# Kernel optimization log

Hardware: AMD Instinct MI355X
Metric: run time of the kernel (lower is better)

The kernel has to match this reference:

```python
import jax, jax.numpy as jnp
import numpy as np

H, W = 48, 48
L = H * W            # 2304 tokens
D = 256              # d_model
NH = 8               # heads (self and memory attn)
FF = 1024            # dim_feedforward
T = 2                # memory frames
BS = 1
GN_GROUPS = 32       # GNActDWConv2d default groups


def layernorm(x, g, b, eps=1e-5):
    m = jnp.mean(x, -1, keepdims=True)
    v = jnp.mean((x - m) ** 2, -1, keepdims=True)
    return (x - m) * jax.lax.rsqrt(v + eps) * g + b


def linear(x, Wt, b):
    # torch nn.Linear convention: Wt is [out, in]
    return x @ Wt.T + b


def mha_core(Q, K, V, nhead):
    # Q [Lq, bs, C], K/V [Lk, bs, C]; AOT MultiheadAttention core (eval: no dropout)
    Lq, bs, C = Q.shape
    hd = C // nhead
    Qh = (Q / np.float32(np.sqrt(hd))).reshape(Lq, bs, nhead, hd).transpose(1, 2, 0, 3)
    Kh = K.reshape(-1, bs, nhead, hd).transpose(1, 2, 0, 3)
    Vh = V.reshape(-1, bs, nhead, hd).transpose(1, 2, 0, 3)
    attn = jax.nn.softmax(jnp.einsum('bhqd,bhkd->bhqk', Qh, Kh), axis=-1)
    out = jnp.einsum('bhqk,bhkd->bhqd', attn, Vh)
    return out.transpose(2, 0, 1, 3).reshape(Lq, bs, C)


def groupnorm(x, g, b, groups, eps=1e-5):
    bs, c, h, w = x.shape
    xg = x.reshape(bs, groups, c // groups, h, w)
    m = jnp.mean(xg, (2, 3, 4), keepdims=True)
    v = jnp.mean((xg - m) ** 2, (2, 3, 4), keepdims=True)
    xg = (xg - m) * jax.lax.rsqrt(v + eps)
    return xg.reshape(bs, c, h, w) * g[None, :, None, None] + b[None, :, None, None]


def dwconv5(x, k):
    # depthwise 5x5, padding=2; x [bs,c,h,w], k [c,1,5,5]
    return jax.lax.conv_general_dilated(x, k, (1, 1), ((2, 2), (2, 2)),
                                        feature_group_count=x.shape[1])


def setup_inputs() -> dict:
    key = jax.random.key(0)
    ks = jax.random.split(key, 16)
    rn = lambda i, shape, s=1.0: jax.random.normal(ks[i], shape, jnp.float32) * s
    w = 0.02
    inp = {
        'tgt': rn(0, (L, BS, D)),
        'global_K': rn(1, (T, L, BS, D)),
        'global_V': rn(2, (T, L, BS, D)),
        'local_K': rn(3, (L, BS, D)),
        'local_V': rn(4, (L, BS, D)),
        # LayerNorms
        'ln1_g': jnp.ones(D, jnp.float32), 'ln1_b': jnp.zeros(D, jnp.float32),
        'ln2_g': jnp.ones(D, jnp.float32), 'ln2_b': jnp.zeros(D, jnp.float32),
        'ln3_g': jnp.ones(D, jnp.float32), 'ln3_b': jnp.zeros(D, jnp.float32),
        'ln4_g': jnp.ones(D, jnp.float32), 'ln4_b': jnp.zeros(D, jnp.float32),
        # self_attn (use_linear=True) Q/K/V + projection
        'sa_Wq': rn(5, (D, D), w), 'sa_bq': jnp.zeros(D, jnp.float32),
        'sa_Wk': rn(6, (D, D), w), 'sa_bk': jnp.zeros(D, jnp.float32),
        'sa_Wv': rn(7, (D, D), w), 'sa_bv': jnp.zeros(D, jnp.float32),
        'sa_Wo': rn(8, (D, D), w), 'sa_bo': jnp.zeros(D, jnp.float32),
        # block linear_Q
        'Wq': rn(9, (D, D), w), 'bq': jnp.zeros(D, jnp.float32),
        # long/short term attn projections (use_linear=False)
        'lt_Wo': rn(10, (D, D), w), 'lt_bo': jnp.zeros(D, jnp.float32),
        'st_Wo': rn(11, (D, D), w), 'st_bo': jnp.zeros(D, jnp.float32),
        # FFN: linear1 -> GN+GELU+DWConv -> linear2
        'W1': rn(12, (FF, D), w), 'b1': jnp.zeros(FF, jnp.float32),
        'gn_g': jnp.ones(FF, jnp.float32), 'gn_b': jnp.zeros(FF, jnp.float32),
        'dw_k': rn(13, (FF, 1, 5, 5), 0.05),
        'W2': rn(14, (D, FF), w), 'b2': jnp.zeros(D, jnp.float32),
    }
    return inp


def reference(tgt, global_K, global_V, local_K, local_V,
              ln1_g, ln1_b, ln2_g, ln2_b, ln3_g, ln3_b, ln4_g, ln4_b,
              sa_Wq, sa_bq, sa_Wk, sa_bk, sa_Wv, sa_bv, sa_Wo, sa_bo,
              Wq, bq, lt_Wo, lt_bo, st_Wo, st_bo,
              W1, b1, gn_g, gn_b, dw_k, W2, b2):
    # --- stage 1: self-attention ---
    _tgt = layernorm(tgt, ln1_g, ln1_b)
    q = linear(_tgt, sa_Wq, sa_bq)
    k = linear(_tgt, sa_Wk, sa_bk)
    v = linear(_tgt, sa_Wv, sa_bv)
    tgt2 = linear(mha_core(q, k, v, NH), sa_Wo, sa_bo)
    tgt = tgt + tgt2  # droppath is identity at eval

    # --- stage 2: long-term + short-term memory cross-attention ---
    _tgt = layernorm(tgt, ln2_g, ln2_b)
    curr_Q = linear(_tgt, Wq, bq)
    curr_K = curr_Q
    curr_V = _tgt

    flat_K = global_K.reshape(-1, BS, D)  # [T*L, bs, D]
    flat_V = global_V.reshape(-1, BS, D)
    tgt2 = linear(mha_core(curr_Q, flat_K, flat_V, NH), lt_Wo, lt_bo)

    k_st = layernorm(local_K + curr_K, ln4_g, ln4_b)
    v_st = layernorm(local_V + curr_V, ln4_g, ln4_b)
    tgt3 = linear(mha_core(curr_Q, k_st, v_st, NH), st_Wo, st_bo)

    tgt = tgt + tgt2 + tgt3

    # --- stage 3: FFN with GN + GELU + depthwise conv ---
    _tgt = layernorm(tgt, ln3_g, ln3_b)
    x = linear(_tgt, W1, b1)                        # [L, bs, FF]
    x = x.reshape(H, W, BS, FF).transpose(2, 3, 0, 1)  # [bs, FF, H, W]
    x = jax.nn.gelu(groupnorm(x, gn_g, gn_b, GN_GROUPS), approximate=False)
    x = dwconv5(x, dw_k)
    x = x.reshape(BS, FF, L).transpose(2, 0, 1)     # [L, bs, FF]
    tgt2 = linear(x, W2, b2)
    return tgt + tgt2
```

## Files before the change

kernel.cpp:

```cpp
#include <hip/hip_runtime.h>
#include <hip/hip_bf16.h>

#define L   2304
#define D   256
#define NHD 8
#define HD  32
#define FF  1024
#define HH  48
#define WWW 48
#define SPL 4
#define RCH 24
#define RP  (L / RCH)
#define S2LOG 0.25503486f

typedef unsigned short bfraw;
typedef __attribute__((ext_vector_type(8))) short s8v;
typedef __attribute__((ext_vector_type(4))) float f4v;

__device__ __forceinline__ bfraw f2b(float x) {
    __hip_bfloat16 h = __float2bfloat16(x);
    return __builtin_bit_cast(bfraw, h);
}

__global__ __launch_bounds__(256) void diag_kernel(float* __restrict__ out, float c, int n)
{
    int i = blockIdx.x * 256 + threadIdx.x;
    if (i < n) out[i] = c;
}

__global__ __launch_bounds__(256) void ln_kernel(
    const float* __restrict__ inA, const float* __restrict__ inB,
    const float* __restrict__ g, const float* __restrict__ b,
    float* __restrict__ out, bfraw* __restrict__ outb)
{
    int row = blockIdx.x, t = threadIdx.x;
    size_t idx = (size_t)row * D + t;
    float v = inA[idx];
    if (inB) v += inB[idx];
    __shared__ float rs[256], rq[256];
    rs[t] = v; rq[t] = v * v;
    __syncthreads();
    for (int o = 128; o > 0; o >>= 1) {
        if (t < o) { rs[t] += rs[t + o]; rq[t] += rq[t + o]; }
        __syncthreads();
    }
    float mean = rs[0] * (1.f / D);
    float var  = rq[0] * (1.f / D) - mean * mean;
    float rstd = rsqrtf(var + 1e-5f);
    float r = (v - mean) * rstd * g[t] + b[t];
    if (out)  out[idx]  = r;
    if (outb) outb[idx] = f2b(r);
}

__global__ __launch_bounds__(256) void ln2_ln4v(
    const float* __restrict__ t5, const float* __restrict__ lV,
    const float* __restrict__ g2, const float* __restrict__ b2,
    const float* __restrict__ g4, const float* __restrict__ b4,
    bfraw* __restrict__ out2b, float* __restrict__ outv)
{
    int row = blockIdx.x, t = threadIdx.x;
    size_t idx = (size_t)row * D + t;
    float v = t5[idx];
    __shared__ float rs[256], rq[256];
    rs[t] = v; rq[t] = v * v;
    __syncthreads();
    for (int o = 128; o > 0; o >>= 1) {
        if (t < o) { rs[t] += rs[t + o]; rq[t] += rq[t + o]; }
        __syncthreads();
    }
    float mean = rs[0] * (1.f / D);
    float var  = rq[0] * (1.f / D) - mean * mean;
    float rstd = rsqrtf(var + 1e-5f);
    float r2 = (v - mean) * rstd * g2[t] + b2[t];
    out2b[idx] = f2b(r2);
    float u = r2 + lV[idx];
    __syncthreads();
    rs[t] = u; rq[t] = u * u;
    __syncthreads();
    for (int o = 128; o > 0; o >>= 1) {
        if (t < o) { rs[t] += rs[t + o]; rq[t] += rq[t + o]; }
        __syncthreads();
    }
    float mean2 = rs[0] * (1.f / D);
    float var2  = rq[0] * (1.f / D) - mean2 * mean2;
    float rstd2 = rsqrtf(var2 + 1e-5f);
    outv[idx] = (u - mean2) * rstd2 * g4[t] + b4[t];
}

__global__ __launch_bounds__(256) void gemm_mfma(
    const bfraw* __restrict__ A, const float* __restrict__ W,
    const float* __restrict__ bias, const float* res, float* out,
    bfraw* __restrict__ outb, float oscale,
    int M, int N, int K)
{
    __shared__ __attribute__((aligned(16))) short Wl[64][32];
    int t = threadIdx.x;
    int w = t >> 6, l = t & 63;
    int lo = l & 15, quad = l >> 4;
    int m0 = blockIdx.x * 32, n0 = blockIdx.y * 64;
    int wr = (w & 1) * 16, wc = (w >> 1) * 32;
    f4v acc[2];
    acc[0] = (f4v){0.f, 0.f, 0.f, 0.f};
    acc[1] = (f4v){0.f, 0.f, 0.f, 0.f};

    int aswz = (quad ^ ((lo >> 2) & 3)) * 8;
    int srow = t >> 3, spart = t & 7;
    const bfraw* ap = A + (size_t)(m0 + wr + lo) * K + quad * 8;

    for (int k0 = 0; k0 < K; k0 += 32) {
        float4 w4[2];
        #pragma unroll
        for (int i = 0; i < 2; i++)
            w4[i] = *reinterpret_cast<const float4*>(W + (size_t)(n0 + i * 32 + srow) * K + k0 + spart * 4);
        s8v af = *reinterpret_cast<const s8v*>(ap + k0);
        __syncthreads();
        #pragma unroll
        for (int i = 0; i < 2; i++) {
            int row = i * 32 + srow;
            int col = ((spart >> 1) ^ ((row >> 2) & 3)) * 8 + (spart & 1) * 4;
            ushort4 wb;
            wb.x = f2b(w4[i].x); wb.y = f2b(w4[i].y); wb.z = f2b(w4[i].z); wb.w = f2b(w4[i].w);
            *reinterpret_cast<ushort4*>(&Wl[row][col]) = wb;
        }
        __syncthreads();
        #pragma unroll
        for (int j = 0; j < 2; j++) {
            int rw = wc + j * 16 + lo;
            s8v wf = *reinterpret_cast<const s8v*>(&Wl[rw][aswz]);
            acc[j] = __builtin_amdgcn_mfma_f32_16x16x32_bf16(af, wf, acc[j], 0, 0, 0);
        }
    }

    #pragma unroll
    for (int j = 0; j < 2; j++) {
        #pragma unroll
        for (int r = 0; r < 4; r++) {
            int mrow = m0 + wr + quad * 4 + r;
            int ncol = n0 + wc + j * 16 + lo;
            float v = acc[j][r] + bias[ncol];
            size_t idx = (size_t)mrow * N + ncol;
            if (res) v += res[idx];
            if (out) out[idx] = v;
            if (outb) outb[idx] = f2b(v * oscale);
        }
    }
}

__global__ __launch_bounds__(256) void gemm_qkv(
    const bfraw* __restrict__ A,
    const float* __restrict__ Wq_, const float* __restrict__ bq_,
    const float* __restrict__ Wk_, const float* __restrict__ bk_,
    const float* __restrict__ Wv_, const float* __restrict__ bv_,
    bfraw* __restrict__ qb, bfraw* __restrict__ kb, bfraw* __restrict__ vtb)
{
    __shared__ __attribute__((aligned(16))) short Wl[64][32];
    int t = threadIdx.x;
    int w = t >> 6, l = t & 63;
    int lo = l & 15, quad = l >> 4;
    int sel = blockIdx.y >> 2;
    int m0 = blockIdx.x * 32, n0 = (blockIdx.y & 3) * 64;
    int wr = (w & 1) * 16, wc = (w >> 1) * 32;
    const float* W    = (sel == 0) ? Wq_ : (sel == 1) ? Wk_ : Wv_;
    const float* bias = (sel == 0) ? bq_ : (sel == 1) ? bk_ : bv_;
    f4v acc[2];
    acc[0] = (f4v){0.f, 0.f, 0.f, 0.f};
    acc[1] = (f4v){0.f, 0.f, 0.f, 0.f};

    int aswz = (quad ^ ((lo >> 2) & 3)) * 8;
    int srow = t >> 3, spart = t & 7;
    const bfraw* ap = A + (size_t)(m0 + wr + lo) * D + quad * 8;

    for (int k0 = 0; k0 < D; k0 += 32) {
        float4 w4[2];
        #pragma unroll
        for (int i = 0; i < 2; i++)
            w4[i] = *reinterpret_cast<const float4*>(W + (size_t)(n0 + i * 32 + srow) * D + k0 + spart * 4);
        s8v af = *reinterpret_cast<const s8v*>(ap + k0);
        __syncthreads();
        #pragma unroll
        for (int i = 0; i < 2; i++) {
            int row = i * 32 + srow;
            int col = ((spart >> 1) ^ ((row >> 2) & 3)) * 8 + (spart & 1) * 4;
            ushort4 wb;
            wb.x = f2b(w4[i].x); wb.y = f2b(w4[i].y); wb.z = f2b(w4[i].z); wb.w = f2b(w4[i].w);
            *reinterpret_cast<ushort4*>(&Wl[row][col]) = wb;
        }
        __syncthreads();
        #pragma unroll
        for (int j = 0; j < 2; j++) {
            int rw = wc + j * 16 + lo;
            s8v wf = *reinterpret_cast<const s8v*>(&Wl[rw][aswz]);
            acc[j] = __builtin_amdgcn_mfma_f32_16x16x32_bf16(af, wf, acc[j], 0, 0, 0);
        }
    }

    #pragma unroll
    for (int j = 0; j < 2; j++) {
        #pragma unroll
        for (int r = 0; r < 4; r++) {
            int mrow = m0 + wr + quad * 4 + r;
            int ncol = n0 + wc + j * 16 + lo;
            float v = acc[j][r] + bias[ncol];
            if (sel == 0)      qb[(size_t)mrow * D + ncol] = f2b(v * S2LOG);
            else if (sel == 1) kb[(size_t)mrow * D + ncol] = f2b(v);
            else               vtb[(size_t)ncol * L + mrow] = f2b(v);
        }
    }
}

__global__ __launch_bounds__(256) void cvtT_kernel(
    const float* __restrict__ in, bfraw* __restrict__ out, int N)
{
    __shared__ float Ls[32][33];
    int h = blockIdx.y, n0 = blockIdx.x * 32, t = threadIdx.x;
    int nl = t >> 3, dq = t & 7;
    float4 v = *reinterpret_cast<const float4*>(in + (size_t)(n0 + nl) * D + h * HD + dq * 4);
    Ls[nl][dq*4+0] = v.x; Ls[nl][dq*4+1] = v.y;
    Ls[nl][dq*4+2] = v.z; Ls[nl][dq*4+3] = v.w;
    __syncthreads();
    int dl = t >> 3, nq = t & 7;
    ushort4 o;
    o.x = f2b(Ls[nq*4+0][dl]); o.y = f2b(Ls[nq*4+1][dl]);
    o.z = f2b(Ls[nq*4+2][dl]); o.w = f2b(Ls[nq*4+3][dl]);
    *reinterpret_cast<ushort4*>(out + (size_t)(h * HD + dl) * N + n0 + nq * 4) = o;
}

__global__ __launch_bounds__(256) void cvt_both(
    const float* __restrict__ gK, bfraw* __restrict__ kb1,
    const float* __restrict__ gV, bfraw* __restrict__ vtb1)
{
    __shared__ float Ls[32][33];
    int t = threadIdx.x;
    if (blockIdx.y < NHD) {
        int h = blockIdx.y, n0 = blockIdx.x * 32;
        const int N = 2 * L;
        int nl = t >> 3, dq = t & 7;
        float4 v = *reinterpret_cast<const float4*>(gV + (size_t)(n0 + nl) * D + h * HD + dq * 4);
        Ls[nl][dq*4+0] = v.x; Ls[nl][dq*4+1] = v.y;
        Ls[nl][dq*4+2] = v.z; Ls[nl][dq*4+3] = v.w;
        __syncthreads();
        int dl = t >> 3, nq = t & 7;
        ushort4 o;
        o.x = f2b(Ls[nq*4+0][dl]); o.y = f2b(Ls[nq*4+1][dl]);
        o.z = f2b(Ls[nq*4+2][dl]); o.w = f2b(Ls[nq*4+3][dl]);
        *reinterpret_cast<ushort4*>(vtb1 + (size_t)(h * HD + dl) * N + n0 + nq * 4) = o;
    } else {
        size_t i = ((size_t)(blockIdx.x * 8 + (blockIdx.y - NHD)) * 256 + t) * 4;
        float4 v = *reinterpret_cast<const float4*>(gK + i);
        ushort4 o;
        o.x = f2b(v.x); o.y = f2b(v.y); o.z = f2b(v.z); o.w = f2b(v.w);
        *reinterpret_cast<ushort4*>(kb1 + i) = o;
    }
}

__global__ __launch_bounds__(256) void attn_mfma_split(
    const bfraw* __restrict__ Qb, const bfraw* __restrict__ Kb,
    const bfraw* __restrict__ Vt, float* __restrict__ OP,
    float* __restrict__ ML, int Lk, int chunk)
{
    __shared__ __attribute__((aligned(16))) short Ks[64][32];
    __shared__ __attribute__((aligned(16))) short Vts[32][72];
    __shared__ __attribute__((aligned(16))) short Ps[4][16][72];
    __shared__ float Tb[4][16][33];
    int t = threadIdx.x;
    int w = t >> 6, l = t & 63;
    int h = blockIdx.y, q0 = blockIdx.x * 64 + w * 16, z = blockIdx.z;
    int lo = l & 15, quad = l >> 4;
    int kb = z * chunk, ke = kb + chunk;

    s8v qf = *reinterpret_cast<const s8v*>(Qb + (size_t)(q0 + lo) * D + h * HD + quad * 8);
    int kswz = (quad ^ ((lo >> 2) & 3)) * 8;

    int skey = t >> 2, spart = t & 3;
    int kcol = (spart ^ ((skey >> 2) & 3)) * 8;
    int sd = t >> 3, svp = t & 7;
    const bfraw* kp = Kb + (size_t)skey * D + h * HD + spart * 8;
    const bfraw* vp = Vt + (size_t)(h * HD + sd) * Lk + svp * 8;

    float m_r = -1e30f, l_r = 0.f;
    f4v o0 = {0.f, 0.f, 0.f, 0.f}, o1 = {0.f, 0.f, 0.f, 0.f};

    for (int k0 = kb; k0 < ke; k0 += 64) {
        s8v kv = *reinterpret_cast<const s8v*>(kp + (size_t)k0 * D);
        s8v vv = *reinterpret_cast<const s8v*>(vp + k0);
        __syncthreads();
        *reinterpret_cast<s8v*>(&Ks[skey][kcol]) = kv;
        *reinterpret_cast<s8v*>(&Vts[sd][svp * 8]) = vv;
        __syncthreads();

        f4v sc4[4];
        #pragma unroll
        for (int s = 0; s < 4; s++) {
            s8v kf = *reinterpret_cast<const s8v*>(&Ks[lo + 16 * s][kswz]);
            sc4[s] = __builtin_amdgcn_mfma_f32_16x16x32_bf16(kf, qf, (f4v){0.f,0.f,0.f,0.f}, 0, 0, 0);
        }
        float cm = -1e30f;
        #pragma unroll
        for (int s = 0; s < 4; s++)
            #pragma unroll
            for (int r = 0; r < 4; r++)
                cm = fmaxf(cm, sc4[s][r]);
        cm = fmaxf(cm, __shfl_xor(cm, 16));
        cm = fmaxf(cm, __shfl_xor(cm, 32));
        bool skip = __all(cm <= m_r + 8.f);
        if (!skip) {
            float mnew = fmaxf(m_r, cm);
            float alpha = __builtin_amdgcn_exp2f(m_r - mnew);
            l_r *= alpha;
            #pragma unroll
            for (int r = 0; r < 4; r++) { o0[r] *= alpha; o1[r] *= alpha; }
            m_r = mnew;
        }
        float ls = 0.f;
        #pragma unroll
        for (int s = 0; s < 4; s++) {
            float p0 = __builtin_amdgcn_exp2f(sc4[s][0] - m_r);
            float p1 = __builtin_amdgcn_exp2f(sc4[s][1] - m_r);
            float p2 = __builtin_amdgcn_exp2f(sc4[s][2] - m_r);
            float p3 = __builtin_amdgcn_exp2f(sc4[s][3] - m_r);
            ls += p0 + p1 + p2 + p3;
            ushort4 pk;
            pk.x = f2b(p0); pk.y = f2b(p1); pk.z = f2b(p2); pk.w = f2b(p3);
            *reinterpret_cast<ushort4*>(&Ps[w][lo][s * 16 + quad * 4]) = pk;
        }
        ls += __shfl_xor(ls, 16);
        ls += __shfl_xor(ls, 32);
        l_r += ls;
        #pragma unroll
        for (int kc = 0; kc < 2; kc++) {
            s8v pf = *reinterpret_cast<const s8v*>(&Ps[w][lo][kc * 32 + quad * 8]);
            s8v v0 = *reinterpret_cast<const s8v*>(&Vts[lo][kc * 32 + quad * 8]);
            s8v v1 = *reinterpret_cast<const s8v*>(&Vts[16 + lo][kc * 32 + quad * 8]);
            o0 = __builtin_amdgcn_mfma_f32_16x16x32_bf16(v0, pf, o0, 0, 0, 0);
            o1 = __builtin_amdgcn_mfma_f32_16x16x32_bf16(v1, pf, o1, 0, 0, 0);
        }
    }

    #pragma unroll
    for (int r = 0; r < 4; r++) {
        Tb[w][lo][quad * 4 + r]      = o0[r];
        Tb[w][lo][16 + quad * 4 + r] = o1[r];
    }
    float* Oz = OP + (size_t)z * L * D;
    int ql = l >> 2, dq = (l & 3) * 8;
    float4 u0, u1;
    u0.x = Tb[w][ql][dq + 0]; u0.y = Tb[w][ql][dq + 1];
    u0.z = Tb[w][ql][dq + 2]; u0.w = Tb[w][ql][dq + 3];
    u1.x = Tb[w][ql][dq + 4]; u1.y = Tb[w][ql][dq + 5];
    u1.z = Tb[w][ql][dq + 6]; u1.w = Tb[w][ql][dq + 7];
    *reinterpret_cast<float4*>(Oz + (size_t)(q0 + ql) * D + h * HD + dq)     = u0;
    *reinterpret_cast<float4*>(Oz + (size_t)(q0 + ql) * D + h * HD + dq + 4) = u1;
    if (l < 16) {
        size_t mi = (((size_t)z * NHD + h) * L + q0 + lo) * 2;
        ML[mi]     = m_r;
        ML[mi + 1] = l_r;
    }
}

__global__ __launch_bounds__(256) void attn_combine(
    const float* __restrict__ OP, const float* __restrict__ ML,
    bfraw* __restrict__ Ob)
{
    int q = blockIdx.x, t = threadIdx.x, h = t >> 5;
    float m[SPL], lv[SPL];
    float M = -1e30f;
    #pragma unroll
    for (int s = 0; s < SPL; s++) {
        size_t mi = (((size_t)s * NHD + h) * L + q) * 2;
        m[s]  = ML[mi];
        lv[s] = ML[mi + 1];
        M = fmaxf(M, m[s]);
    }
    float wl = 0.f, acc = 0.f;
    #pragma unroll
    for (int s = 0; s < SPL; s++) {
        float w = __builtin_amdgcn_exp2f(m[s] - M);
        wl  += w * lv[s];
        acc += w * OP[(size_t)s * L * D + (size_t)q * D + t];
    }
    Ob[(size_t)q * D + t] = f2b(acc / wl);
}

__global__ __launch_bounds__(256) void gn_stats_part(
    const float* __restrict__ X, float* __restrict__ ps)
{
    int g = blockIdx.x, rc = blockIdx.y, t = threadIdx.x;
    int cq = (t & 7) * 4;
    int rl = t >> 3;
    int r0 = rc * RP;
    float s = 0.f, sq = 0.f;
    #pragma unroll
    for (int p = 0; p < RP / 32; p++) {
        int l = r0 + p * 32 + rl;
        float4 v = *reinterpret_cast<const float4*>(X + (size_t)l * FF + g * 32 + cq);
        s  += v.x + v.y + v.z + v.w;
        sq += v.x*v.x + v.y*v.y + v.z*v.z + v.w*v.w;
    }
    __shared__ float rs[256], rq[256];
    rs[t] = s; rq[t] = sq;
    __syncthreads();
    for (int o = 128; o > 0; o >>= 1) {
        if (t < o) { rs[t] += rs[t + o]; rq[t] += rq[t + o]; }
        __syncthreads();
    }
    if (t == 0) {
        ps[(g * RCH + rc) * 2]     = rs[0];
        ps[(g * RCH + rc) * 2 + 1] = rq[0];
    }
}

__global__ __launch_bounds__(256) void gn_gelu_dwconv(
    const float* __restrict__ X, const float* __restrict__ ps,
    const float* __restrict__ gg, const float* __restrict__ gb,
    const float* __restrict__ Kw, bfraw* __restrict__ Y)
{
    __shared__ float tile[144][64];
    int h0 = blockIdx.x * 8, w0 = blockIdx.y * 8, c0 = blockIdx.z * 64;
    int t = threadIdx.x;
    int c = t & 63;
    int cg = (c0 + c) >> 5;
    float s = 0.f, sq = 0.f;
    #pragma unroll
    for (int i = 0; i < RCH; i++) {
        s  += ps[(cg * RCH + i) * 2];
        sq += ps[(cg * RCH + i) * 2 + 1];
    }
    float n = (float)(L * 32);
    float mu = s / n;
    float rs = rsqrtf(sq / n - mu * mu + 1e-5f);
    float ga = gg[c0 + c], be = gb[c0 + c];

    for (int i = t; i < 144 * 64; i += 256) {
        int sp = i >> 6;
        int hy = h0 + (sp / 12) - 2, wx = w0 + (sp % 12) - 2;
        float v = 0.f;
        if (hy >= 0 && hy < HH && wx >= 0 && wx < WWW) {
            float x = X[(size_t)(hy * WWW + wx) * FF + c0 + c];
            x = (x - mu) * rs * ga + be;
            v = 0.5f * x * (1.f + erff(x * 0.70710678118654752f));
        }
        tile[sp][c] = v;
    }
    float kw[25];
    #pragma unroll
    for (int i = 0; i < 25; i++) kw[i] = Kw[(size_t)(c0 + c) * 25 + i];
    __syncthreads();

    int sgrp = t >> 6;
    for (int sIdx = 0; sIdx < 16; sIdx++) {
        int sp = sgrp * 16 + sIdx;
        int oh = sp >> 3, ow = sp & 7;
        float acc = 0.f;
        #pragma unroll
        for (int ky = 0; ky < 5; ky++)
            #pragma unroll
            for (int kx = 0; kx < 5; kx++)
                acc += tile[(oh + ky) * 12 + ow + kx][c] * kw[ky * 5 + kx];
        Y[(size_t)((h0 + oh) * WWW + w0 + ow) * FF + c0 + c] = f2b(acc);
    }
}

extern "C" void kernel_launch(void* const* d_in, const int* in_sizes, int n_in,
                              void* d_out, int out_size, void* d_ws, size_t ws_size,
                              hipStream_t stream)
{
    (void)in_sizes;
    float* out = (float*)d_out;

    if (n_in != 34) {
        diag_kernel<<<(out_size + 255) / 256, 256, 0, stream>>>(out, 2000.f, out_size);
        return;
    }

    const float* tgt    = (const float*)d_in[0];
    const float* gK     = (const float*)d_in[1];
    const float* gV     = (const float*)d_in[2];
    const float* lK     = (const float*)d_in[3];
    const float* lV     = (const float*)d_in[4];
    const float* ln1_g  = (const float*)d_in[5];
    const float* ln1_b  = (const float*)d_in[6];
    const float* ln2_g  = (const float*)d_in[7];
    const float* ln2_b  = (const float*)d_in[8];
    const float* ln3_g  = (const float*)d_in[9];
    const float* ln3_b  = (const float*)d_in[10];
    const float* ln4_g  = (const float*)d_in[11];
    const float* ln4_b  = (const float*)d_in[12];
    const float* sa_Wq  = (const float*)d_in[13];
    const float* sa_bq  = (const float*)d_in[14];
    const float* sa_Wk  = (const float*)d_in[15];
    const float* sa_bk  = (const float*)d_in[16];
    const float* sa_Wv  = (const float*)d_in[17];
    const float* sa_bv  = (const float*)d_in[18];
    const float* sa_Wo  = (const float*)d_in[19];
    const float* sa_bo  = (const float*)d_in[20];
    const float* Wq     = (const float*)d_in[21];
    const float* bq     = (const float*)d_in[22];
    const float* lt_Wo  = (const float*)d_in[23];
    const float* lt_bo  = (const float*)d_in[24];
    const float* st_Wo  = (const float*)d_in[25];
    const float* st_bo  = (const float*)d_in[26];
    const float* W1w    = (const float*)d_in[27];
    const float* b1w    = (const float*)d_in[28];
    const float* gn_g   = (const float*)d_in[29];
    const float* gn_b   = (const float*)d_in[30];
    const float* dw_k   = (const float*)d_in[31];
    const float* W2w    = (const float*)d_in[32];
    const float* b2w    = (const float*)d_in[33];

    const size_t LD = (size_t)L * D;
    const size_t NEED = (6 * LD + (size_t)L * FF + 64) * 4;
    float* ws = (float*)d_ws;
    float* t0 = ws + 0 * LD;
    float* t1 = ws + 1 * LD;
    float* t3 = ws + 3 * LD;
    float* t4 = ws + 4 * LD;
    float* t5 = ws + 5 * LD;
    float* X1 = t0;
    float* X2 = ws + 6 * LD;
    bfraw* qb   = (bfraw*)X2;
    bfraw* kb1  = qb + LD;
    bfraw* vtb1 = qb + 3 * LD;
    bfraw* kb2  = qb + 5 * LD;
    bfraw* vtb2 = qb + 6 * LD;
    float* OP   = ws;
    float* ML   = X2 + (7 * LD) / 2;
    float* PS   = ML;
    bfraw* t0b  = (bfraw*)t0;
    bfraw* t3b  = (bfraw*)t3;
    bfraw* t4b  = (bfraw*)t4;
    bfraw* X2b  = (bfraw*)X2;

    if (ws_size < NEED) {
        int wsMiB = (int)(ws_size >> 20); if (wsMiB > 63) wsMiB = 63;
        diag_kernel<<<(out_size + 255) / 256, 256, 0, stream>>>(out, 64.f + (float)wsMiB, out_size);
        return;
    }

    dim3 gDD(L / 32, D / 64);
    dim3 gDF(L / 32, FF / 64);
    dim3 gQKV(L / 32, 12);
    dim3 gATS(L / 64, NHD, SPL);
    dim3 gT1(L / 32, NHD);
    dim3 gCB(2 * L / 32, NHD + 8);
    dim3 gGN(32, RCH);
    dim3 gDW(6, 6, 16);

    ln_kernel<<<L, 256, 0, stream>>>(tgt, nullptr, ln1_g, ln1_b, nullptr, t0b);
    gemm_qkv<<<gQKV, 256, 0, stream>>>(t0b, sa_Wq, sa_bq, sa_Wk, sa_bk, sa_Wv, sa_bv,
                                       qb, kb2, vtb2);
    attn_mfma_split<<<gATS, 256, 0, stream>>>(qb, kb2, vtb2, OP, ML, L, L / SPL);
    attn_combine<<<L, 256, 0, stream>>>(OP, ML, t4b);
    gemm_mfma<<<gDD, 256, 0, stream>>>(t4b, sa_Wo, sa_bo, tgt, t5, nullptr, 1.f, L, D, D);

    ln2_ln4v<<<L, 256, 0, stream>>>(t5, lV, ln2_g, ln2_b, ln4_g, ln4_b, t3b, t0);
    gemm_mfma<<<gDD, 256, 0, stream>>>(t3b, Wq, bq, nullptr, t1, qb, S2LOG, L, D, D);
    ln_kernel<<<L, 256, 0, stream>>>(t1, lK, ln4_g, ln4_b, nullptr, kb2);
    cvtT_kernel<<<gT1, 256, 0, stream>>>(t0, vtb2, L);
    cvt_both<<<gCB, 256, 0, stream>>>(gK, kb1, gV, vtb1);
    attn_mfma_split<<<gATS, 256, 0, stream>>>(qb, kb1, vtb1, OP, ML, 2 * L, 2 * L / SPL);
    attn_combine<<<L, 256, 0, stream>>>(OP, ML, t4b);
    gemm_mfma<<<gDD, 256, 0, stream>>>(t4b, lt_Wo, lt_bo, t5, t5, nullptr, 1.f, L, D, D);
    attn_mfma_split<<<gATS, 256, 0, stream>>>(qb, kb2, vtb2, OP, ML, L, L / SPL);
    attn_combine<<<L, 256, 0, stream>>>(OP, ML, t4b);
    gemm_mfma<<<gDD, 256, 0, stream>>>(t4b, st_Wo, st_bo, t5, t5, nullptr, 1.f, L, D, D);

    ln_kernel<<<L, 256, 0, stream>>>(t5, nullptr, ln3_g, ln3_b, nullptr, t4b);
    gemm_mfma<<<gDF, 256, 0, stream>>>(t4b, W1w, b1w, nullptr, X1, nullptr, 1.f, L, FF, D);
    gn_stats_part<<<gGN, 256, 0, stream>>>(X1, PS);
    gn_gelu_dwconv<<<gDW, 256, 0, stream>>>(X1, PS, gn_g, gn_b, dw_k, X2b);
    gemm_mfma<<<gDD, 256, 0, stream>>>(X2b, W2w, b2w, t5, out, nullptr, 1.f, L, D, FF);
}
```

Before: 338.2 us.

## Fuse long- and short-term memory attention, combine, and output projections into single launches

Runs the long-term and short-term cross-attention in one launch. The z-dimension picks the memory, and each memory uses two key splits instead of four. Their combines are merged into one kernel, and the two output projections are fused into a dual-GEMM that accumulates both into one result with both biases and the residual. The key layernorm and the V transpose-convert are also merged into one launch. This cuts launch count and the extra round trips through the residual buffer, but it lowers split parallelism for the long-term attention (2 splits over 2L keys) and needs new workspace aliasing.

```diff
diff --git a/kernel.cpp b/kernel.cpp
--- a/kernel.cpp
+++ b/kernel.cpp
@@ -87,6 +87,45 @@
     outv[idx] = (u - mean2) * rstd2 * g4[t] + b4[t];
 }
 
+__global__ __launch_bounds__(256) void ln_cvtT(
+    const float* __restrict__ t1, const float* __restrict__ lK,
+    const float* __restrict__ g4, const float* __restrict__ b4,
+    bfraw* __restrict__ kb2,
+    const float* __restrict__ vsrc, bfraw* __restrict__ vtb2)
+{
+    __shared__ float rs[256], rq[256];
+    __shared__ float Ls[32][33];
+    int t = threadIdx.x;
+    if (blockIdx.x < L) {
+        int row = blockIdx.x;
+        size_t idx = (size_t)row * D + t;
+        float v = t1[idx] + lK[idx];
+        rs[t] = v; rq[t] = v * v;
+        __syncthreads();
+        for (int o = 128; o > 0; o >>= 1) {
+            if (t < o) { rs[t] += rs[t + o]; rq[t] += rq[t + o]; }
+            __syncthreads();
+        }
+        float mean = rs[0] * (1.f / D);
+        float var  = rq[0] * (1.f / D) - mean * mean;
+        float rstd = rsqrtf(var + 1e-5f);
+        kb2[idx] = f2b((v - mean) * rstd * g4[t] + b4[t]);
+    } else {
+        int idx = blockIdx.x - L;
+        int n0 = (idx >> 3) * 32, h = idx & 7;
+        int nl = t >> 3, dq = t & 7;
+        float4 v = *reinterpret_cast<const float4*>(vsrc + (size_t)(n0 + nl) * D + h * HD + dq * 4);
+        Ls[nl][dq*4+0] = v.x; Ls[nl][dq*4+1] = v.y;
+        Ls[nl][dq*4+2] = v.z; Ls[nl][dq*4+3] = v.w;
+        __syncthreads();
+        int dl = t >> 3, nq = t & 7;
+        ushort4 o;
+        o.x = f2b(Ls[nq*4+0][dl]); o.y = f2b(Ls[nq*4+1][dl]);
+        o.z = f2b(Ls[nq*4+2][dl]); o.w = f2b(Ls[nq*4+3][dl]);
+        *reinterpret_cast<ushort4*>(vtb2 + (size_t)(h * HD + dl) * L + n0 + nq * 4) = o;
+    }
+}
+
 __global__ __launch_bounds__(256) void gemm_mfma(
     const bfraw* __restrict__ A, const float* __restrict__ W,
     const float* __restrict__ bias, const float* res, float* out,
@@ -142,6 +181,65 @@
             if (res) v += res[idx];
             if (out) out[idx] = v;
             if (outb) outb[idx] = f2b(v * oscale);
+        }
+    }
+}
+
+__global__ __launch_bounds__(256) void gemm_dual(
+    const bfraw* __restrict__ A1, const float* __restrict__ W1, const float* __restrict__ b1,
+    const bfraw* __restrict__ A2, const float* __restrict__ W2, const float* __restrict__ b2,
+    const float* __restrict__ res, float* __restrict__ out)
+{
+    __shared__ __attribute__((aligned(16))) short Wl[64][32];
+    int t = threadIdx.x;
+    int w = t >> 6, l = t & 63;
+    int lo = l & 15, quad = l >> 4;
+    int m0 = blockIdx.x * 32, n0 = blockIdx.y * 64;
+    int wr = (w & 1) * 16, wc = (w >> 1) * 32;
+    f4v acc[2];
+    acc[0] = (f4v){0.f, 0.f, 0.f, 0.f};
+    acc[1] = (f4v){0.f, 0.f, 0.f, 0.f};
+
+    int aswz = (quad ^ ((lo >> 2) & 3)) * 8;
+    int srow = t >> 3, spart = t & 7;
+
+    #pragma unroll
+    for (int half = 0; half < 2; half++) {
+        const bfraw* ap = (half ? A2 : A1) + (size_t)(m0 + wr + lo) * D + quad * 8;
+        const float* W  = half ? W2 : W1;
+        for (int k0 = 0; k0 < D; k0 += 32) {
+            float4 w4[2];
+            #pragma unroll
+            for (int i = 0; i < 2; i++)
+                w4[i] = *reinterpret_cast<const float4*>(W + (size_t)(n0 + i * 32 + srow) * D + k0 + spart * 4);
+            s8v af = *reinterpret_cast<const s8v*>(ap + k0);
+            __syncthreads();
+            #pragma unroll
+            for (int i = 0; i < 2; i++) {
+                int row = i * 32 + srow;
+                int col = ((spart >> 1) ^ ((row >> 2) & 3)) * 8 + (spart & 1) * 4;
+                ushort4 wb;
+                wb.x = f2b(w4[i].x); wb.y = f2b(w4[i].y); wb.z = f2b(w4[i].z); wb.w = f2b(w4[i].w);
+                *reinterpret_cast<ushort4*>(&Wl[row][col]) = wb;
+            }
+            __syncthreads();
+            #pragma unroll
+            for (int j = 0; j < 2; j++) {
+                int rw = wc + j * 16 + lo;
+                s8v wf = *reinterpret_cast<const s8v*>(&Wl[rw][aswz]);
+                acc[j] = __builtin_amdgcn_mfma_f32_16x16x32_bf16(af, wf, acc[j], 0, 0, 0);
+            }
+        }
+    }
+
+    #pragma unroll
+    for (int j = 0; j < 2; j++) {
+        #pragma unroll
+        for (int r = 0; r < 4; r++) {
+            int mrow = m0 + wr + quad * 4 + r;
+            int ncol = n0 + wc + j * 16 + lo;
+            size_t idx = (size_t)mrow * D + ncol;
+            out[idx] = acc[j][r] + b1[ncol] + b2[ncol] + res[idx];
         }
     }
 }
@@ -208,23 +306,6 @@
     }
 }
 
-__global__ __launch_bounds__(256) void cvtT_kernel(
-    const float* __restrict__ in, bfraw* __restrict__ out, int N)
-{
-    __shared__ float Ls[32][33];
-    int h = blockIdx.y, n0 = blockIdx.x * 32, t = threadIdx.x;
-    int nl = t >> 3, dq = t & 7;
-    float4 v = *reinterpret_cast<const float4*>(in + (size_t)(n0 + nl) * D + h * HD + dq * 4);
-    Ls[nl][dq*4+0] = v.x; Ls[nl][dq*4+1] = v.y;
-    Ls[nl][dq*4+2] = v.z; Ls[nl][dq*4+3] = v.w;
-    __syncthreads();
-    int dl = t >> 3, nq = t & 7;
-    ushort4 o;
-    o.x = f2b(Ls[nq*4+0][dl]); o.y = f2b(Ls[nq*4+1][dl]);
-    o.z = f2b(Ls[nq*4+2][dl]); o.w = f2b(Ls[nq*4+3][dl]);
-    *reinterpret_cast<ushort4*>(out + (size_t)(h * HD + dl) * N + n0 + nq * 4) = o;
-}
-
 __global__ __launch_bounds__(256) void cvt_both(
     const float* __restrict__ gK, bfraw* __restrict__ kb1,
     const float* __restrict__ gV, bfraw* __restrict__ vtb1)
@@ -253,20 +334,17 @@
     }
 }
 
-__global__ __launch_bounds__(256) void attn_mfma_split(
+__device__ __forceinline__ void attn_core(
     const bfraw* __restrict__ Qb, const bfraw* __restrict__ Kb,
     const bfraw* __restrict__ Vt, float* __restrict__ OP,
-    float* __restrict__ ML, int Lk, int chunk)
-{
-    __shared__ __attribute__((aligned(16))) short Ks[64][32];
-    __shared__ __attribute__((aligned(16))) short Vts[32][72];
-    __shared__ __attribute__((aligned(16))) short Ps[4][16][72];
-    __shared__ float Tb[4][16][33];
+    float* __restrict__ ML, int Lk, int chunk, int zz,
+    short (*Ks)[32], short (*Vts)[72], short (*Ps)[72], float (*Tb)[33])
+{
     int t = threadIdx.x;
     int w = t >> 6, l = t & 63;
-    int h = blockIdx.y, q0 = blockIdx.x * 64 + w * 16, z = blockIdx.z;
+    int h = blockIdx.y, q0 = blockIdx.x * 64 + w * 16;
     int lo = l & 15, quad = l >> 4;
-    int kb = z * chunk, ke = kb + chunk;
+    int kb = zz * chunk, ke = kb + chunk;
 
     s8v qf = *reinterpret_cast<const s8v*>(Qb + (size_t)(q0 + lo) * D + h * HD + quad * 8);
     int kswz = (quad ^ ((lo >> 2) & 3)) * 8;
@@ -321,14 +399,14 @@
             ls += p0 + p1 + p2 + p3;
             ushort4 pk;
             pk.x = f2b(p0); pk.y = f2b(p1); pk.z = f2b(p2); pk.w = f2b(p3);
-            *reinterpret_cast<ushort4*>(&Ps[w][lo][s * 16 + quad * 4]) = pk;
+            *reinterpret_cast<ushort4*>(&Ps[lo][s * 16 + quad * 4]) = pk;
         }
         ls += __shfl_xor(ls, 16);
         ls += __shfl_xor(ls, 32);
         l_r += ls;
         #pragma unroll
         for (int kc = 0; kc < 2; kc++) {
-            s8v pf = *reinterpret_cast<const s8v*>(&Ps[w][lo][kc * 32 + quad * 8]);
+            s8v pf = *reinterpret_cast<const s8v*>(&Ps[lo][kc * 32 + quad * 8]);
             s8v v0 = *reinterpret_cast<const s8v*>(&Vts[lo][kc * 32 + quad * 8]);
             s8v v1 = *reinterpret_cast<const s8v*>(&Vts[16 + lo][kc * 32 + quad * 8]);
             o0 = __builtin_amdgcn_mfma_f32_16x16x32_bf16(v0, pf, o0, 0, 0, 0);
@@ -338,23 +416,55 @@
 
     #pragma unroll
     for (int r = 0; r < 4; r++) {
-        Tb[w][lo][quad * 4 + r]      = o0[r];
-        Tb[w][lo][16 + quad * 4 + r] = o1[r];
-    }
-    float* Oz = OP + (size_t)z * L * D;
+        Tb[lo][quad * 4 + r]      = o0[r];
+        Tb[lo][16 + quad * 4 + r] = o1[r];
+    }
+    float* Oz = OP + (size_t)zz * L * D;
     int ql = l >> 2, dq = (l & 3) * 8;
     float4 u0, u1;
-    u0.x = Tb[w][ql][dq + 0]; u0.y = Tb[w][ql][dq + 1];
-    u0.z = Tb[w][ql][dq + 2]; u0.w = Tb[w][ql][dq + 3];
-    u1.x = Tb[w][ql][dq + 4]; u1.y = Tb[w][ql][dq + 5];
-    u1.z = Tb[w][ql][dq + 6]; u1.w = Tb[w][ql][dq + 7];
+    u0.x = Tb[ql][dq + 0]; u0.y = Tb[ql][dq + 1];
+    u0.z = Tb[ql][dq + 2]; u0.w = Tb[ql][dq + 3];
+    u1.x = Tb[ql][dq + 4]; u1.y = Tb[ql][dq + 5];
+    u1.z = Tb[ql][dq + 6]; u1.w = Tb[ql][dq + 7];
     *reinterpret_cast<float4*>(Oz + (size_t)(q0 + ql) * D + h * HD + dq)     = u0;
     *reinterpret_cast<float4*>(Oz + (size_t)(q0 + ql) * D + h * HD + dq + 4) = u1;
     if (l < 16) {
-        size_t mi = (((size_t)z * NHD + h) * L + q0 + lo) * 2;
+        size_t mi = (((size_t)zz * NHD + h) * L + q0 + lo) * 2;
         ML[mi]     = m_r;
         ML[mi + 1] = l_r;
     }
+}
+
+__global__ __launch_bounds__(256) void attn_mfma_split(
+    const bfraw* __restrict__ Qb, const bfraw* __restrict__ Kb,
+    const bfraw* __restrict__ Vt, float* __restrict__ OP,
+    float* __restrict__ ML, int Lk, int chunk)
+{
+    __shared__ __attribute__((aligned(16))) short Ks[64][32];
+    __shared__ __attribute__((aligned(16))) short Vts[32][72];
+    __shared__ __attribute__((aligned(16))) short Ps[4][16][72];
+    __shared__ float Tb[4][16][33];
+    int w = threadIdx.x >> 6;
+    attn_core(Qb, Kb, Vt, OP, ML, Lk, chunk, blockIdx.z, Ks, Vts, Ps[w], Tb[w]);
+}
+
+__global__ __launch_bounds__(256) void attn_ltst(
+    const bfraw* __restrict__ Qb,
+    const bfraw* __restrict__ K_lt, const bfraw* __restrict__ V_lt,
+    float* __restrict__ OP_lt, float* __restrict__ ML_lt,
+    const bfraw* __restrict__ K_st, const bfraw* __restrict__ V_st,
+    float* __restrict__ OP_st, float* __restrict__ ML_st)
+{
+    __shared__ __attribute__((aligned(16))) short Ks[64][32];
+    __shared__ __attribute__((aligned(16))) short Vts[32][72];
+    __shared__ __attribute__((aligned(16))) short Ps[4][16][72];
+    __shared__ float Tb[4][16][33];
+    int w = threadIdx.x >> 6;
+    int z = blockIdx.z;
+    if (z < 2)
+        attn_core(Qb, K_lt, V_lt, OP_lt, ML_lt, 2 * L, L, z, Ks, Vts, Ps[w], Tb[w]);
+    else
+        attn_core(Qb, K_st, V_st, OP_st, ML_st, L, L / 2, z - 2, Ks, Vts, Ps[w], Tb[w]);
 }
 
 __global__ __launch_bounds__(256) void attn_combine(
@@ -374,6 +484,32 @@
     float wl = 0.f, acc = 0.f;
     #pragma unroll
     for (int s = 0; s < SPL; s++) {
+        float w = __builtin_amdgcn_exp2f(m[s] - M);
+        wl  += w * lv[s];
+        acc += w * OP[(size_t)s * L * D + (size_t)q * D + t];
+    }
+    Ob[(size_t)q * D + t] = f2b(acc / wl);
+}
+
+__global__ __launch_bounds__(256) void combine2_both(
+    const float* __restrict__ OP_lt, const float* __restrict__ ML_lt, bfraw* __restrict__ Ob_lt,
+    const float* __restrict__ OP_st, const float* __restrict__ ML_st, bfraw* __restrict__ Ob_st)
+{
+    int q = blockIdx.x, t = threadIdx.x, h = t >> 5;
+    const float* OP = blockIdx.y ? OP_st : OP_lt;
+    const float* ML = blockIdx.y ? ML_st : ML_lt;
+    bfraw* Ob = blockIdx.y ? Ob_st : Ob_lt;
+    float m[2], lv[2];
+    #pragma unroll
+    for (int s = 0; s < 2; s++) {
+        size_t mi = (((size_t)s * NHD + h) * L + q) * 2;
+        m[s]  = ML[mi];
+        lv[s] = ML[mi + 1];
+    }
+    float M = fmaxf(m[0], m[1]);
+    float wl = 0.f, acc = 0.f;
+    #pragma unroll
+    for (int s = 0; s < 2; s++) {
         float w = __builtin_amdgcn_exp2f(m[s] - M);
         wl  += w * lv[s];
         acc += w * OP[(size_t)s * L * D + (size_t)q * D + t];
@@ -512,6 +648,7 @@
     float* ws = (float*)d_ws;
     float* t0 = ws + 0 * LD;
     float* t1 = ws + 1 * LD;
+    float* t2 = ws + 2 * LD;
     float* t3 = ws + 3 * LD;
     float* t4 = ws + 4 * LD;
     float* t5 = ws + 5 * LD;
@@ -523,11 +660,17 @@
     bfraw* kb2  = qb + 5 * LD;
     bfraw* vtb2 = qb + 6 * LD;
     float* OP   = ws;
+    float* OPlt = t0;
+    float* OPst = t2;
     float* ML   = X2 + (7 * LD) / 2;
+    float* MLlt = ML;
+    float* MLst = ML + 2 * (size_t)NHD * L * 2;
     float* PS   = ML;
     bfraw* t0b  = (bfraw*)t0;
     bfraw* t3b  = (bfraw*)t3;
     bfraw* t4b  = (bfraw*)t4;
+    bfraw* obLT = t4b;
+    bfraw* obST = t4b + LD;
     bfraw* X2b  = (bfraw*)X2;
 
     if (ws_size < NEED) {
@@ -540,8 +683,9 @@
     dim3 gDF(L / 32, FF / 64);
     dim3 gQKV(L / 32, 12);
     dim3 gATS(L / 64, NHD, SPL);
-    dim3 gT1(L / 32, NHD);
+    dim3 gAT2(L / 64, NHD, 4);
     dim3 gCB(2 * L / 32, NHD + 8);
+    dim3 gC2(L, 2);
     dim3 gGN(32, RCH);
     dim3 gDW(6, 6, 16);
 
@@ -554,15 +698,11 @@
 
     ln2_ln4v<<<L, 256, 0, stream>>>(t5, lV, ln2_g, ln2_b, ln4_g, ln4_b, t3b, t0);
     gemm_mfma<<<gDD, 256, 0, stream>>>(t3b, Wq, bq, nullptr, t1, qb, S2LOG, L, D, D);
-    ln_kernel<<<L, 256, 0, stream>>>(t1, lK, ln4_g, ln4_b, nullptr, kb2);
-    cvtT_kernel<<<gT1, 256, 0, stream>>>(t0, vtb2, L);
+    ln_cvtT<<<L + (L / 32) * NHD, 256, 0, stream>>>(t1, lK, ln4_g, ln4_b, kb2, t0, vtb2);
     cvt_both<<<gCB, 256, 0, stream>>>(gK, kb1, gV, vtb1);
-    attn_mfma_split<<<gATS, 256, 0, stream>>>(qb, kb1, vtb1, OP, ML, 2 * L, 2 * L / SPL);
-    attn_combine<<<L, 256, 0, stream>>>(OP, ML, t4b);
-    gemm_mfma<<<gDD, 256, 0, stream>>>(t4b, lt_Wo, lt_bo, t5, t5, nullptr, 1.f, L, D, D);
-    attn_mfma_split<<<gATS, 256, 0, stream>>>(qb, kb2, vtb2, OP, ML, L, L / SPL);
-    attn_combine<<<L, 256, 0, stream>>>(OP, ML, t4b);
-    gemm_mfma<<<gDD, 256, 0, stream>>>(t4b, st_Wo, st_bo, t5, t5, nullptr, 1.f, L, D, D);
+    attn_ltst<<<gAT2, 256, 0, stream>>>(qb, kb1, vtb1, OPlt, MLlt, kb2, vtb2, OPst, MLst);
+    combine2_both<<<gC2, 256, 0, stream>>>(OPlt, MLlt, obLT, OPst, MLst, obST);
+    gemm_dual<<<gDD, 256, 0, stream>>>(obLT, lt_Wo, lt_bo, obST, st_Wo, st_bo, t5, t5);
 
     ln_kernel<<<L, 256, 0, stream>>>(t5, nullptr, ln3_g, ln3_b, nullptr, t4b);
     gemm_mfma<<<gDF, 256, 0, stream>>>(t4b, W1w, b1w, nullptr, X1, nullptr, 1.f, L, FF, D);
```

Result: faster. 320.1 us (-5.4%).
